# Kernel optimization log

Measured on AMD Instinct MI355X. Metric: run time of the kernel, lower is better.

Reference implementation:

```python
import jax, jax.numpy as jnp
import numpy as np

N = 16384
D = 512
VOCAB = 100000
EMB_SCALE = 0.05  # keep dot products ~O(1) so exp() is stable, like trained embeddings


def setup_inputs() -> dict:
    key = jax.random.key(0)
    k1, k2, k3, k4 = jax.random.split(key, 4)
    input_emb = jax.random.normal(k1, (N, D), dtype=jnp.float32) * EMB_SCALE
    target_emb = jax.random.normal(k2, (N, D), dtype=jnp.float32) * EMB_SCALE
    target_ids = jax.random.randint(k3, (N,), 0, VOCAB, dtype=jnp.int64) if jax.config.jax_enable_x64 else jax.random.randint(k3, (N,), 0, VOCAB, dtype=jnp.int32)
    # sampling probabilities in (eps, ~0.5) so 1 - q stays well away from 0
    q_probas = jax.random.uniform(k4, (N,), dtype=jnp.float32, minval=1e-4, maxval=0.5)
    # first half positives, second half negatives (static pattern, matches boolean-mask semantics)
    mask = jnp.arange(N) < (N // 2)
    return {"input_emb": input_emb, "target_emb": target_emb, "target_ids": target_ids,
            "q_probas": q_probas, "mask": mask}


def reference(input_emb, target_emb, target_ids, q_probas, mask):
    # mask is a constant selection pattern -> resolve to static index lists (jit-friendly shapes)
    mask_np = np.asarray(mask)
    pos_idx = np.nonzero(mask_np)[0]
    neg_idx = np.nonzero(~mask_np)[0]

    pos_emb = input_emb[pos_idx]                      # [P, D]
    pos_tgt = target_emb[pos_idx]                     # [P, D]
    neg_tgt = target_emb[neg_idx]                     # [Q, D]

    pos_sim = jnp.einsum('pd,pd->p', pos_emb, pos_tgt)          # [P]
    neg_sim = jnp.einsum('pd,qd->pq', pos_emb, neg_tgt)         # [P, Q]

    # accidental-hit mask: 1 where negative id differs from the positive's true id
    miss = (target_ids[pos_idx][:, None] != target_ids[neg_idx]).astype(jnp.float32)  # [P, Q]
    n_miss = jnp.sum(miss, axis=1, keepdims=True)                # [P, 1]

    # logQ correction: subtract log(n_miss * q_neg / (1 - q_pos))
    log_q = jnp.log(n_miss * q_probas[neg_idx][None, :] / (1.0 - q_probas[pos_idx][:, None]))
    neg_exp = jnp.exp(neg_sim - log_q)                           # [P, Q]
    neg_exp_sum = jnp.einsum('pq,pq->p', miss, neg_exp)          # [P]

    pos_exp = jnp.exp(pos_sim)
    batch_loss = jnp.mean(-pos_sim + jnp.log(pos_exp + neg_exp_sum))
    return batch_loss
```

## Files before the change

kernel.cpp:

```cpp
#include <hip/hip_runtime.h>
#include <hip/hip_bf16.h>

#define NPOS 8192
#define NNEG 8192
#define DIM  512
#define VOCAB 100000

#define FP8_SCALE 64.0f
#define ACC_DESCALE (1.0f / 4096.0f)

typedef float f32x4 __attribute__((ext_vector_type(4)));
typedef long  lng2  __attribute__((ext_vector_type(2)));

__device__ __forceinline__ void async_load16(const void* g, void* l) {
    __builtin_amdgcn_global_load_lds(
        (const __attribute__((address_space(1))) void*)g,
        (__attribute__((address_space(3))) void*)l, 16, 0, 0);
}

__global__ void prep_kernel(const float* __restrict__ input_emb,
                            const float* __restrict__ target_emb,
                            const int* __restrict__ ids,
                            const float* __restrict__ q_probas,
                            unsigned char* __restrict__ A8,
                            unsigned char* __restrict__ B8,
                            float* __restrict__ w, float* __restrict__ pos_sim,
                            int* __restrict__ hist) {
    const int r    = (blockIdx.x * blockDim.x + threadIdx.x) >> 6;
    const int lane = threadIdx.x & 63;

    const float4* ain = (const float4*)(input_emb  + (size_t)r * DIM);
    const float4* tin = (const float4*)(target_emb + (size_t)r * DIM);
    const float4* bin = (const float4*)(target_emb + (size_t)(NPOS + r) * DIM);

    float4 a0 = ain[lane * 2], a1 = ain[lane * 2 + 1];
    float4 t0 = tin[lane * 2], t1 = tin[lane * 2 + 1];
    float4 b0 = bin[lane * 2], b1 = bin[lane * 2 + 1];

    int alo = __builtin_amdgcn_cvt_pk_fp8_f32(a0.x * FP8_SCALE, a0.y * FP8_SCALE, 0, false);
    alo     = __builtin_amdgcn_cvt_pk_fp8_f32(a0.z * FP8_SCALE, a0.w * FP8_SCALE, alo, true);
    int ahi = __builtin_amdgcn_cvt_pk_fp8_f32(a1.x * FP8_SCALE, a1.y * FP8_SCALE, 0, false);
    ahi     = __builtin_amdgcn_cvt_pk_fp8_f32(a1.z * FP8_SCALE, a1.w * FP8_SCALE, ahi, true);
    int blo = __builtin_amdgcn_cvt_pk_fp8_f32(b0.x * FP8_SCALE, b0.y * FP8_SCALE, 0, false);
    blo     = __builtin_amdgcn_cvt_pk_fp8_f32(b0.z * FP8_SCALE, b0.w * FP8_SCALE, blo, true);
    int bhi = __builtin_amdgcn_cvt_pk_fp8_f32(b1.x * FP8_SCALE, b1.y * FP8_SCALE, 0, false);
    bhi     = __builtin_amdgcn_cvt_pk_fp8_f32(b1.z * FP8_SCALE, b1.w * FP8_SCALE, bhi, true);

    const int s = lane & 7, wnd = lane >> 3;
    const int phys = wnd * 64 + (s & 3) * 16 + (s >> 2) * 8;
    *(int2*)(A8 + (size_t)r * DIM + phys) = make_int2(alo, ahi);
    *(int2*)(B8 + (size_t)r * DIM + phys) = make_int2(blo, bhi);

    float sum = a0.x * t0.x + a0.y * t0.y + a0.z * t0.z + a0.w * t0.w
              + a1.x * t1.x + a1.y * t1.y + a1.z * t1.z + a1.w * t1.w;
    #pragma unroll
    for (int m = 32; m >= 1; m >>= 1) sum += __shfl_xor(sum, m);

    if (lane == 0) {
        pos_sim[r] = sum;
        w[r] = 1.0f / q_probas[NPOS + r];
        atomicAdd(&hist[ids[NPOS + r]], 1);
    }
}

__global__ __launch_bounds__(512) void gemm_kernel(
        const unsigned char* __restrict__ A8, const unsigned char* __restrict__ B8,
        const int* __restrict__ ids, const float* __restrict__ w,
        float* __restrict__ S) {
    __shared__ __align__(16) unsigned char Atile[2][128 * 64];
    __shared__ __align__(16) unsigned char Btile[2][128 * 64];

    const int tid  = threadIdx.x;
    const int lane = tid & 63;
    const int wv   = tid >> 6;
    const int wave_m = (wv & 1) * 64;
    const int wave_n = (wv >> 1) * 32;
    const int quad = lane >> 4;
    const int r16  = lane & 15;
    const int bm = blockIdx.x, bn = blockIdx.y;

    f32x4 acc[4][2] = {};

    const int u     = wv & 3;
    const bool isB  = wv >= 4;
    const int sgran = (lane & 3) ^ ((lane >> 3) & 3);
    const size_t goff0 = (size_t)(u * 32 + (lane >> 2)) * DIM + sgran * 16;
    const size_t goff1 = (size_t)(u * 32 + 16 + (lane >> 2)) * DIM + sgran * 16;
    const unsigned char* a_src = A8 + (size_t)(bm * 128) * DIM;
    const unsigned char* b_src = B8 + (size_t)(bn * 128) * DIM;
    const unsigned char* src = isB ? b_src : a_src;
    const int ldst0 = (u * 2) * 1024;
    const int ldst1 = (u * 2 + 1) * 1024;

    {
        unsigned char* tb = isB ? Btile[0] : Atile[0];
        async_load16(src + goff0, tb + ldst0);
        async_load16(src + goff1, tb + ldst1);
    }
    __syncthreads();

    const int slot = quad ^ ((r16 >> 1) & 3);
    for (int it = 0; it < 8; ++it) {
        const int cur = it & 1;
        if (it < 7) {
            const size_t kb = (size_t)(it + 1) * 64;
            unsigned char* tb = isB ? Btile[cur ^ 1] : Atile[cur ^ 1];
            async_load16(src + kb + goff0, tb + ldst0);
            async_load16(src + kb + goff1, tb + ldst1);
        }

        lng2 af[4], bg[2];
        #pragma unroll
        for (int i = 0; i < 4; ++i) {
            const int arow = wave_m + i * 16 + r16;
            af[i] = *(const lng2*)(Atile[cur] + arow * 64 + slot * 16);
        }
        #pragma unroll
        for (int j = 0; j < 2; ++j) {
            const int brow = wave_n + j * 16 + r16;
            bg[j] = *(const lng2*)(Btile[cur] + brow * 64 + slot * 16);
        }
        #pragma unroll
        for (int i = 0; i < 4; ++i)
            #pragma unroll
            for (int j = 0; j < 2; ++j)
                acc[i][j] = __builtin_amdgcn_mfma_f32_16x16x32_fp8_fp8(af[i].x, bg[j].x, acc[i][j], 0, 0, 0);
        #pragma unroll
        for (int i = 0; i < 4; ++i)
            #pragma unroll
            for (int j = 0; j < 2; ++j)
                acc[i][j] = __builtin_amdgcn_mfma_f32_16x16x32_fp8_fp8(af[i].y, bg[j].y, acc[i][j], 0, 0, 0);

        if (it < 7) __syncthreads();
    }

    int idq[2]; float wq[2];
    #pragma unroll
    for (int j = 0; j < 2; ++j) {
        const int q = bn * 128 + wave_n + j * 16 + r16;
        idq[j] = ids[NPOS + q];
        wq[j]  = w[q];
    }
    #pragma unroll
    for (int i = 0; i < 4; ++i) {
        const int p0 = bm * 128 + wave_m + i * 16 + quad * 4;
        #pragma unroll
        for (int rr = 0; rr < 4; ++rr) {
            const int p = p0 + rr;
            const int idp = ids[p];
            float partial = 0.f;
            #pragma unroll
            for (int j = 0; j < 2; ++j) {
                const float e = __expf(acc[i][j][rr] * ACC_DESCALE) * wq[j];
                partial += (idp != idq[j]) ? e : 0.f;
            }
            partial += __shfl_xor(partial, 1);
            partial += __shfl_xor(partial, 2);
            partial += __shfl_xor(partial, 4);
            partial += __shfl_xor(partial, 8);
            if (r16 == 0) atomicAdd(&S[p], partial);
        }
    }
}

__global__ __launch_bounds__(1024) void final_kernel(
        const float* __restrict__ pos_sim,
        const float* __restrict__ S,
        const int* __restrict__ hist,
        const int* __restrict__ ids,
        const float* __restrict__ q_probas,
        float* __restrict__ out) {
    __shared__ float red[16];
    float local = 0.f;
    #pragma unroll
    for (int k = 0; k < 8; ++k) {
        const int p = k * 1024 + threadIdx.x;
        const float ps  = pos_sim[p];
        const float n_miss = (float)(NNEG - hist[ids[p]]);
        const float nes = S[p] * (1.0f - q_probas[p]) / n_miss;
        local += -ps + logf(expf(ps) + nes);
    }
    #pragma unroll
    for (int m = 32; m >= 1; m >>= 1) local += __shfl_xor(local, m);
    if ((threadIdx.x & 63) == 0) red[threadIdx.x >> 6] = local;
    __syncthreads();
    if (threadIdx.x < 16) {
        float v = red[threadIdx.x];
        #pragma unroll
        for (int m = 8; m >= 1; m >>= 1) v += __shfl_xor(v, m, 16);
        if (threadIdx.x == 0) out[0] = v / (float)NPOS;
    }
}

extern "C" void kernel_launch(void* const* d_in, const int* in_sizes, int n_in,
                              void* d_out, int out_size, void* d_ws, size_t ws_size,
                              hipStream_t stream) {
    const float* input_emb  = (const float*)d_in[0];
    const float* target_emb = (const float*)d_in[1];
    const int*   target_ids = (const int*)d_in[2];
    const float* q_probas   = (const float*)d_in[3];

    char* ws = (char*)d_ws;
    unsigned char* A8 = (unsigned char*)ws;
    unsigned char* B8 = (unsigned char*)(ws + (size_t)NPOS * DIM);
    float*  S       = (float*)(ws + (size_t)NPOS * DIM * 2);
    int*    hist    = (int*)(S + NPOS);
    float*  w       = (float*)(hist + VOCAB);
    float*  pos_sim = w + NPOS;

    hipMemsetAsync(S, 0, (size_t)(NPOS + VOCAB) * 4, stream);
    prep_kernel<<<2048, 256, 0, stream>>>(input_emb, target_emb, target_ids,
                                          q_probas, A8, B8, w, pos_sim, hist);
    gemm_kernel<<<dim3(64, 64), 512, 0, stream>>>(A8, B8, target_ids, w, S);
    final_kernel<<<1, 1024, 0, stream>>>(pos_sim, S, hist, target_ids, q_probas, (float*)d_out);
}
```

Measured before the change: 195.1 us.

## Load GEMM fragments directly from global memory instead of LDS double-buffering

Removes the LDS double-buffered async tile loads and barriers from the FP8 GEMM kernel. Each wave now reads its MFMA operand fragments straight from global memory (relying on L1/L2 for reuse across waves), with the K loop fully unrolled. This eliminates LDS traffic and __syncthreads, but loses explicit sharing of tiles between the 8 waves, so global/L2 load traffic goes up. It also drops the prefetch overlap.

```diff
diff --git a/kernel.cpp b/kernel.cpp
--- a/kernel.cpp
+++ b/kernel.cpp
@@ -11,12 +11,6 @@
 
 typedef float f32x4 __attribute__((ext_vector_type(4)));
 typedef long  lng2  __attribute__((ext_vector_type(2)));
-
-__device__ __forceinline__ void async_load16(const void* g, void* l) {
-    __builtin_amdgcn_global_load_lds(
-        (const __attribute__((address_space(1))) void*)g,
-        (__attribute__((address_space(3))) void*)l, 16, 0, 0);
-}
 
 __global__ void prep_kernel(const float* __restrict__ input_emb,
                             const float* __restrict__ target_emb,
@@ -67,9 +61,6 @@
         const unsigned char* __restrict__ A8, const unsigned char* __restrict__ B8,
         const int* __restrict__ ids, const float* __restrict__ w,
         float* __restrict__ S) {
-    __shared__ __align__(16) unsigned char Atile[2][128 * 64];
-    __shared__ __align__(16) unsigned char Btile[2][128 * 64];
-
     const int tid  = threadIdx.x;
     const int lane = tid & 63;
     const int wv   = tid >> 6;
@@ -81,45 +72,23 @@
 
     f32x4 acc[4][2] = {};
 
-    const int u     = wv & 3;
-    const bool isB  = wv >= 4;
-    const int sgran = (lane & 3) ^ ((lane >> 3) & 3);
-    const size_t goff0 = (size_t)(u * 32 + (lane >> 2)) * DIM + sgran * 16;
-    const size_t goff1 = (size_t)(u * 32 + 16 + (lane >> 2)) * DIM + sgran * 16;
-    const unsigned char* a_src = A8 + (size_t)(bm * 128) * DIM;
-    const unsigned char* b_src = B8 + (size_t)(bn * 128) * DIM;
-    const unsigned char* src = isB ? b_src : a_src;
-    const int ldst0 = (u * 2) * 1024;
-    const int ldst1 = (u * 2 + 1) * 1024;
+    const unsigned char* ap[4];
+    const unsigned char* bp[2];
+    #pragma unroll
+    for (int i = 0; i < 4; ++i)
+        ap[i] = A8 + (size_t)(bm * 128 + wave_m + i * 16 + r16) * DIM + quad * 16;
+    #pragma unroll
+    for (int j = 0; j < 2; ++j)
+        bp[j] = B8 + (size_t)(bn * 128 + wave_n + j * 16 + r16) * DIM + quad * 16;
 
-    {
-        unsigned char* tb = isB ? Btile[0] : Atile[0];
-        async_load16(src + goff0, tb + ldst0);
-        async_load16(src + goff1, tb + ldst1);
-    }
-    __syncthreads();
-
-    const int slot = quad ^ ((r16 >> 1) & 3);
+    #pragma unroll
     for (int it = 0; it < 8; ++it) {
-        const int cur = it & 1;
-        if (it < 7) {
-            const size_t kb = (size_t)(it + 1) * 64;
-            unsigned char* tb = isB ? Btile[cur ^ 1] : Atile[cur ^ 1];
-            async_load16(src + kb + goff0, tb + ldst0);
-            async_load16(src + kb + goff1, tb + ldst1);
-        }
-
         lng2 af[4], bg[2];
         #pragma unroll
-        for (int i = 0; i < 4; ++i) {
-            const int arow = wave_m + i * 16 + r16;
-            af[i] = *(const lng2*)(Atile[cur] + arow * 64 + slot * 16);
-        }
+        for (int i = 0; i < 4; ++i) af[i] = *(const lng2*)(ap[i] + it * 64);
         #pragma unroll
-        for (int j = 0; j < 2; ++j) {
-            const int brow = wave_n + j * 16 + r16;
-            bg[j] = *(const lng2*)(Btile[cur] + brow * 64 + slot * 16);
-        }
+        for (int j = 0; j < 2; ++j) bg[j] = *(const lng2*)(bp[j] + it * 64);
+
         #pragma unroll
         for (int i = 0; i < 4; ++i)
             #pragma unroll
@@ -130,8 +99,6 @@
             #pragma unroll
             for (int j = 0; j < 2; ++j)
                 acc[i][j] = __builtin_amdgcn_mfma_f32_16x16x32_fp8_fp8(af[i].y, bg[j].y, acc[i][j], 0, 0, 0);
-
-        if (it < 7) __syncthreads();
     }
 
     int idq[2]; float wq[2];
```

New measurement: 325.6 us. +66.9%, slower.
